# Performance work log

Hardware: AMD Instinct MI355X
Metric: run time of the kernel (lower is better)

Reference implementation:

```python
import jax, jax.numpy as jnp
import numpy as np

# Gemma3-style config
B, S, HID = 2, 2048, 2560      # 2 sequences of 2048 tokens (flattened ragged prefill, equal lengths)
H, KV, D = 8, 4, 256           # attention heads, kv heads (GQA groups=2), head_dim
WINDOW = 1024                  # sliding window (is_sliding=True)
EPS = 1e-6
SCALE = 256.0 ** -0.5          # query_pre_attn_scalar ** -0.5
ROPE_BASE = 10000.0            # rope_local_base_freq for sliding layers


def setup_inputs() -> dict:
    key = jax.random.key(0)
    ks = jax.random.split(key, 5)
    T = B * S
    hidden_states = jax.random.normal(ks[0], (T, HID), jnp.float32)
    # real rotary tables: positions restart per sequence
    inv_freq = 1.0 / (ROPE_BASE ** (np.arange(0, D, 2, dtype=np.float64) / D))  # [D/2]
    pos = np.tile(np.arange(S, dtype=np.float64), B)                             # [T]
    ang = pos[:, None] * inv_freq[None, :]                                       # [T, D/2]
    cos = jnp.asarray(np.cos(ang), jnp.float32)
    sin = jnp.asarray(np.sin(ang), jnp.float32)
    w_qkv = jax.random.normal(ks[1], ((H + 2 * KV) * D, HID), jnp.float32) * 0.02
    q_norm_w = 1.0 + jax.random.normal(ks[2], (D,), jnp.float32) * 0.02  # Gemma stores weight-1, loads +1
    k_norm_w = 1.0 + jax.random.normal(ks[3], (D,), jnp.float32) * 0.02
    w_o = jax.random.normal(ks[4], (HID, H * D), jnp.float32) * 0.02
    return dict(hidden_states=hidden_states, cos=cos, sin=sin, w_qkv=w_qkv,
                q_norm_w=q_norm_w, k_norm_w=k_norm_w, w_o=w_o)


def _rmsnorm(x, w):
    # per-head RMSNorm in fp32, as Gemma3FastRMSNorm. x: [T, h, D]
    xf = x.astype(jnp.float32)
    var = jnp.mean(xf * xf, axis=-1, keepdims=True)
    return (xf * jax.lax.rsqrt(var + EPS) * w).astype(x.dtype)


def _rope(x, cos, sin):
    # neox-style rotary: rotate across head_dim halves. x: [T, h, D]; cos/sin: [T, D/2]
    x1, x2 = x[..., : D // 2], x[..., D // 2:]
    c, s = cos[:, None, :], sin[:, None, :]
    return jnp.concatenate([x1 * c - x2 * s, x2 * c + x1 * s], axis=-1)


def reference(hidden_states, cos, sin, w_qkv, q_norm_w, k_norm_w, w_o):
    T = hidden_states.shape[0]
    qkv = hidden_states @ w_qkv.T                              # [T, (H+2KV)*D]
    q = qkv[:, : H * D].reshape(T, H, D)
    k = qkv[:, H * D: (H + KV) * D].reshape(T, KV, D)
    v = qkv[:, (H + KV) * D:].reshape(T, KV, D)
    q = _rmsnorm(q, q_norm_w)
    k = _rmsnorm(k, k_norm_w)
    q = _rope(q, cos, sin)
    k = _rope(k, cos, sin)
    # unflatten ragged tokens into [B, S, h, D] (equal-length prefill)
    qb = q.reshape(B, S, H, D)
    kb = jnp.repeat(k.reshape(B, S, KV, D), H // KV, axis=2)   # GQA expand
    vb = jnp.repeat(v.reshape(B, S, KV, D), H // KV, axis=2)
    scores = jnp.einsum('bqhd,bkhd->bhqk', qb, kb) * SCALE     # [B, H, S, S]
    i = jnp.arange(S)[:, None]
    j = jnp.arange(S)[None, :]
    mask = (j <= i) & ((i - j) < WINDOW)                       # causal + sliding window
    scores = jnp.where(mask, scores, jnp.float32(-1e30))
    p = jax.nn.softmax(scores, axis=-1)
    attn = jnp.einsum('bhqk,bkhd->bqhd', p, vb)                # [B, S, H, D]
    attn = attn.reshape(T, H * D)
    return attn @ w_o.T                                        # [T, HID]
```

## Files before the change

### kernel.cpp

```cpp
#include <hip/hip_runtime.h>
#include <cstdint>
#include <cstddef>

#define T_TOK 4096
#define HIDDIM 2560
#define NH 8
#define NKV 4
#define HD 256
#define SEQ 2048
#define NBATCH 2
#define WIN 1024
#define NQKV 4096
#define QSCALE 0.0625f

typedef unsigned short u16;
typedef __attribute__((ext_vector_type(8))) __bf16 bf16x8;
typedef __attribute__((ext_vector_type(8))) u16 u16x8;
typedef __attribute__((ext_vector_type(4))) float f32x4;

__device__ __forceinline__ u16 f2bf(float f) {
  union { float f; uint32_t u; } x{f};
  uint32_t r = x.u + 0x7FFFu + ((x.u >> 16) & 1u);
  return (u16)(r >> 16);
}
__device__ __forceinline__ float bf2f(u16 h) {
  union { uint32_t u; float f; } x{((uint32_t)h) << 16};
  return x.f;
}
__device__ __forceinline__ void gload_lds16(const void* g, void* l) {
  __builtin_amdgcn_global_load_lds((const __attribute__((address_space(1))) unsigned int*)g,
                                   (__attribute__((address_space(3))) unsigned int*)l, 16, 0, 0);
}
template <int N>
__device__ __forceinline__ void vmcnt_wait() {
  if constexpr (N >= 8) asm volatile("s_waitcnt vmcnt(8)" ::: "memory");
  else if constexpr (N == 6) asm volatile("s_waitcnt vmcnt(6)" ::: "memory");
  else if constexpr (N == 4) asm volatile("s_waitcnt vmcnt(4)" ::: "memory");
  else if constexpr (N == 3) asm volatile("s_waitcnt vmcnt(3)" ::: "memory");
  else asm volatile("s_waitcnt vmcnt(0)" ::: "memory");
}

__global__ void cvt_bf16(const float* __restrict__ in, u16* __restrict__ out, int n8) {
  int i = blockIdx.x * 256 + threadIdx.x;
  if (i >= n8) return;
  const f32x4* p = (const f32x4*)(in + (size_t)i * 8);
  f32x4 a = p[0], b = p[1];
  u16 o[8];
  o[0] = f2bf(a[0]); o[1] = f2bf(a[1]); o[2] = f2bf(a[2]); o[3] = f2bf(a[3]);
  o[4] = f2bf(b[0]); o[5] = f2bf(b[1]); o[6] = f2bf(b[2]); o[7] = f2bf(b[3]);
  *(u16x8*)(out + (size_t)i * 8) = *(const u16x8*)o;
}

template <int M, int N, int K, int BN, int OUTBF16>
__global__ __launch_bounds__(512, 2) void gemm256(const u16* __restrict__ A,
                                                  const u16* __restrict__ Bt,
                                                  void* __restrict__ Cp) {
  constexpr int NT = K / 32;
  constexpr int BCH = BN * 4;
  constexpr int LPT = (1024 + BCH) / 512;
  constexpr int NREP = BN / 64;
  constexpr int BUFB = 16384 + BN * 64;
  __shared__ char smem[4 * BUFB];

  const int tid = threadIdx.x, lane = tid & 63, w = tid >> 6;
  const int wr = w >> 2, wc = w & 3, hi = lane >> 4, lo = lane & 15;
  const int hi16 = hi * 16;
  constexpr int TOT = (M / 256) * (N / BN);
  const int bid = blockIdx.x;
  const int wg = (bid & 7) * (TOT / 8) + (bid >> 3);
  const int m0 = (wg / (N / BN)) * 256;
  const int n0 = (wg % (N / BN)) * BN;

  f32x4 acc[8][NREP] = {};

  auto stage = [&](int tt, int bb) {
    const int k0 = tt * 32;
    char* base = smem + bb * BUFB;
#pragma unroll
    for (int it = 0; it < 2; ++it) {
      int c = tid + it * 512;
      int r = (c >> 2) ^ ((c >> 4) & 1);
      int h = (c & 3) ^ (r & 3);
      gload_lds16(A + (size_t)(m0 + r) * K + k0 + h * 8, base + c * 16);
    }
#pragma unroll
    for (int it = 0; it < BCH / 512; ++it) {
      int c = tid + it * 512;
      int r = (c >> 2) ^ ((c >> 4) & 1);
      int h = (c & 3) ^ (r & 3);
      gload_lds16(Bt + (size_t)(n0 + r) * K + k0 + h * 8, base + 16384 + c * 16);
    }
  };
  auto body = [&](int bb) {
    char* base = smem + bb * BUFB;
    bf16x8 a[8], b[NREP];
#pragma unroll
    for (int mi = 0; mi < 8; ++mi) {
      int r = wr * 128 + mi * 16 + lo;
      a[mi] = *(const bf16x8*)(base + ((r * 64 + hi16) ^ ((r & 7) << 4)));
    }
#pragma unroll
    for (int ni = 0; ni < NREP; ++ni) {
      int r = wc * (BN / 4) + ni * 16 + lo;
      b[ni] = *(const bf16x8*)(base + 16384 + ((r * 64 + hi16) ^ ((r & 7) << 4)));
    }
    __builtin_amdgcn_s_setprio(1);
#pragma unroll
    for (int mi = 0; mi < 8; ++mi)
#pragma unroll
      for (int ni = 0; ni < NREP; ++ni)
        acc[mi][ni] = __builtin_amdgcn_mfma_f32_16x16x32_bf16(a[mi], b[ni], acc[mi][ni], 0, 0, 0);
    __builtin_amdgcn_s_setprio(0);
  };

  stage(0, 0); stage(1, 1); stage(2, 2);
  vmcnt_wait<2 * LPT>();
  __builtin_amdgcn_s_barrier();
  int t = 0;
  for (; t < NT - 3; ++t) {
    stage(t + 3, (t + 3) & 3);
    body(t & 3);
    vmcnt_wait<2 * LPT>();
    __builtin_amdgcn_s_barrier();
  }
  body(t & 3); vmcnt_wait<LPT>(); __builtin_amdgcn_s_barrier(); ++t;
  body(t & 3); vmcnt_wait<0>();   __builtin_amdgcn_s_barrier(); ++t;
  body(t & 3);

#pragma unroll
  for (int mi = 0; mi < 8; ++mi)
#pragma unroll
    for (int ni = 0; ni < NREP; ++ni) {
      int row = m0 + wr * 128 + mi * 16 + hi * 4;
      int col = n0 + wc * (BN / 4) + ni * 16 + lo;
#pragma unroll
      for (int r = 0; r < 4; ++r) {
        if (OUTBF16)
          ((u16*)Cp)[(size_t)(row + r) * N + col] = f2bf(acc[mi][ni][r]);
        else
          ((float*)Cp)[(size_t)(row + r) * N + col] = acc[mi][ni][r];
      }
    }
}

__global__ void norm_rope(const u16* __restrict__ qkv, const float* __restrict__ cosb,
                          const float* __restrict__ sinb, const float* __restrict__ qw,
                          const float* __restrict__ kw, u16* __restrict__ qn,
                          u16* __restrict__ kn) {
  int gw = blockIdx.x * 4 + (threadIdx.x >> 6);
  int lane = threadIdx.x & 63;
  int t = gw / 12, hh = gw % 12;
  const u16* x = qkv + (size_t)t * NQKV + hh * HD;
  int d = lane * 2;
  float x1a = bf2f(x[d]), x1b = bf2f(x[d + 1]);
  float x2a = bf2f(x[d + 128]), x2b = bf2f(x[d + 129]);
  float ss = x1a * x1a + x1b * x1b + x2a * x2a + x2b * x2b;
#pragma unroll
  for (int off = 1; off < 64; off <<= 1) ss += __shfl_xor(ss, off, 64);
  float inv = rsqrtf(ss * (1.0f / 256.0f) + 1e-6f);
  const float* wp = (hh < 8) ? qw : kw;
  float c0 = cosb[t * 128 + d], c1 = cosb[t * 128 + d + 1];
  float s0 = sinb[t * 128 + d], s1 = sinb[t * 128 + d + 1];
  float sc = (hh < 8) ? QSCALE : 1.0f;
  float y1a = x1a * inv * wp[d], y1b = x1b * inv * wp[d + 1];
  float y2a = x2a * inv * wp[d + 128], y2b = x2b * inv * wp[d + 129];
  float o1a = (y1a * c0 - y2a * s0) * sc, o1b = (y1b * c1 - y2b * s1) * sc;
  float o2a = (y2a * c0 + y1a * s0) * sc, o2b = (y2b * c1 + y1b * s1) * sc;
  u16* o = (hh < 8) ? (qn + ((size_t)t * 8 + hh) * HD) : (kn + ((size_t)t * 4 + (hh - 8)) * HD);
  ushort2 lo2, hi2;
  lo2.x = f2bf(o1a); lo2.y = f2bf(o1b);
  hi2.x = f2bf(o2a); hi2.y = f2bf(o2b);
  *(ushort2*)&o[d] = lo2;
  *(ushort2*)&o[d + 128] = hi2;
}

__global__ void vtransp(const u16* __restrict__ qkv, u16* __restrict__ vt) {
  const int b = blockIdx.y >> 2, kv = blockIdx.y & 3;
  const int s0 = blockIdx.x * 64;
  const int t = threadIdx.x;
  __shared__ u16 tile[64 * 64];
  for (int d0 = 0; d0 < 256; d0 += 64) {
#pragma unroll
    for (int it = 0; it < 2; ++it) {
      int c = t + it * 256;
      int sr = c >> 3, dc = (c & 7) * 8;
      bf16x8 v = *(const bf16x8*)&qkv[(size_t)(b * SEQ + s0 + sr) * NQKV + 3072 + kv * HD + d0 + dc];
      *(bf16x8*)((char*)tile + ((sr * 128 + dc * 2) ^ ((sr & 7) << 4))) = v;
    }
    __syncthreads();
#pragma unroll
    for (int it = 0; it < 2; ++it) {
      int c = t + it * 256;
      int dr = c >> 3, sc0 = (c & 7) * 8;
      union { u16 a[8]; bf16x8 v; } u;
#pragma unroll
      for (int j = 0; j < 8; ++j) {
        int s = sc0 + j;
        u.a[j] = *(const u16*)((char*)tile + ((s * 128 + dr * 2) ^ ((s & 7) << 4)));
      }
      *(bf16x8*)&vt[((size_t)(b * 4 + kv) * 256 + d0 + dr) * SEQ + s0 + sc0] = u.v;
    }
    __syncthreads();
  }
}

__global__ __launch_bounds__(256, 2) void attn_fwd(const u16* __restrict__ qn,
                                                   const u16* __restrict__ kn,
                                                   const u16* __restrict__ vt,
                                                   u16* __restrict__ aout) {
  const int qt = blockIdx.x * 64, h = blockIdx.y, b = blockIdx.z;
  const int kvh = h >> 1;
  const int t = threadIdx.x, lane = t & 63, w = t >> 6, hi = lane >> 4, lo = lane & 15;
  __shared__ u16 Ks[32 * 256];
  __shared__ u16 Vs[256 * 32];
  __shared__ u16 Ps[4][16 * 32];
  bf16x8 qf[8];
  const int qrow = qt + w * 16 + lo;
#pragma unroll
  for (int dd = 0; dd < 8; ++dd)
    qf[dd] = *(const bf16x8*)&qn[((size_t)(b * SEQ + qrow) * 8 + h) * HD + dd * 32 + hi * 8];
  f32x4 oacc[16] = {};
  float mrow[4] = {-3e38f, -3e38f, -3e38f, -3e38f};
  float lrow[4] = {0.f, 0.f, 0.f, 0.f};
  const int kstart = qt >= WIN ? qt - WIN : 0;
  const int irow = qt + w * 16 + hi * 4;
  for (int kt = kstart; kt < qt + 64; kt += 32) {
#pragma unroll
    for (int it = 0; it < 4; ++it) {
      int c = t + it * 256;
      int kr = c >> 5, dc = (c & 31) * 8;
      bf16x8 val = *(const bf16x8*)&kn[((size_t)(b * SEQ + kt + kr) * 4 + kvh) * HD + dc];
      *(bf16x8*)((char*)Ks + ((kr * 512 + dc * 2) ^ ((kr & 7) << 4))) = val;
    }
#pragma unroll
    for (int it = 0; it < 4; ++it) {
      int c = t + it * 256;
      int dr = c >> 2, kc = (c & 3) * 8;
      bf16x8 val = *(const bf16x8*)&vt[((size_t)(b * 4 + kvh) * 256 + dr) * SEQ + kt + kc];
      *(bf16x8*)((char*)Vs + ((dr * 64 + kc * 2) ^ ((dr & 7) << 4))) = val;
    }
    __syncthreads();
    f32x4 sacc[2];
#pragma unroll
    for (int kk = 0; kk < 2; ++kk) {
      f32x4 sa = {0.f, 0.f, 0.f, 0.f};
#pragma unroll
      for (int dd = 0; dd < 8; ++dd) {
        int krow = kk * 16 + lo;
        bf16x8 kf = *(const bf16x8*)((char*)Ks + ((krow * 512 + (dd * 32 + hi * 8) * 2) ^ ((krow & 7) << 4)));
        sa = __builtin_amdgcn_mfma_f32_16x16x32_bf16(qf[dd], kf, sa, 0, 0, 0);
      }
      sacc[kk] = sa;
    }
    float pe[2][4];
    float tmax[4] = {-3e38f, -3e38f, -3e38f, -3e38f};
#pragma unroll
    for (int kk = 0; kk < 2; ++kk)
#pragma unroll
      for (int r = 0; r < 4; ++r) {
        int i = irow + r, j = kt + kk * 16 + lo;
        bool ok = (j <= i) && (i - j < WIN);
        float sv = ok ? sacc[kk][r] : -3e38f;
        sacc[kk][r] = sv;
        tmax[r] = fmaxf(tmax[r], sv);
      }
#pragma unroll
    for (int off = 1; off < 16; off <<= 1)
#pragma unroll
      for (int r = 0; r < 4; ++r) tmax[r] = fmaxf(tmax[r], __shfl_xor(tmax[r], off, 64));
    float scl[4], tsum[4];
#pragma unroll
    for (int r = 0; r < 4; ++r) {
      float mnew = fmaxf(mrow[r], tmax[r]);
      scl[r] = __expf(mrow[r] - mnew);
      mrow[r] = mnew;
      tsum[r] = 0.f;
    }
#pragma unroll
    for (int kk = 0; kk < 2; ++kk)
#pragma unroll
      for (int r = 0; r < 4; ++r) {
        float sv = sacc[kk][r];
        float p = (sv <= -1e37f) ? 0.f : __expf(sv - mrow[r]);
        pe[kk][r] = p;
        tsum[r] += p;
      }
#pragma unroll
    for (int off = 1; off < 16; off <<= 1)
#pragma unroll
      for (int r = 0; r < 4; ++r) tsum[r] += __shfl_xor(tsum[r], off, 64);
#pragma unroll
    for (int r = 0; r < 4; ++r) lrow[r] = lrow[r] * scl[r] + tsum[r];
#pragma unroll
    for (int dt = 0; dt < 16; ++dt)
#pragma unroll
      for (int r = 0; r < 4; ++r) oacc[dt][r] *= scl[r];
#pragma unroll
    for (int kk = 0; kk < 2; ++kk)
#pragma unroll
      for (int r = 0; r < 4; ++r) {
        int q = hi * 4 + r, cc = kk * 16 + lo;
        *(u16*)((char*)&Ps[w][0] + ((q * 64 + cc * 2) ^ ((q & 7) << 4))) = f2bf(pe[kk][r]);
      }
    bf16x8 pf = *(const bf16x8*)((char*)&Ps[w][0] + ((lo * 64 + hi * 16) ^ ((lo & 7) << 4)));
#pragma unroll
    for (int dt = 0; dt < 16; ++dt) {
      int d = dt * 16 + lo;
      bf16x8 vf = *(const bf16x8*)((char*)Vs + ((d * 64 + hi * 16) ^ ((d & 7) << 4)));
      oacc[dt] = __builtin_amdgcn_mfma_f32_16x16x32_bf16(pf, vf, oacc[dt], 0, 0, 0);
    }
    __syncthreads();
  }
#pragma unroll
  for (int dt = 0; dt < 16; ++dt)
#pragma unroll
    for (int r = 0; r < 4; ++r) {
      int i = irow + r;
      aout[(size_t)(b * SEQ + i) * 2048 + h * HD + dt * 16 + lo] = f2bf(oacc[dt][r] / lrow[r]);
    }
}

extern "C" void kernel_launch(void* const* d_in, const int* in_sizes, int n_in,
                              void* d_out, int out_size, void* d_ws, size_t ws_size,
                              hipStream_t stream) {
  const float* hs = (const float*)d_in[0];
  const float* cosb = (const float*)d_in[1];
  const float* sinb = (const float*)d_in[2];
  const float* wqkv = (const float*)d_in[3];
  const float* qw = (const float*)d_in[4];
  const float* kw = (const float*)d_in[5];
  const float* wo = (const float*)d_in[6];
  char* ws = (char*)d_ws;
  u16* hs_b = (u16*)(ws);
  u16* wqkv_b = (u16*)(ws + 20971520);
  u16* wo_b = (u16*)(ws + 41943040);
  u16* qkv_b = (u16*)(ws + 52428800);
  u16* kn = (u16*)(ws + 85983232);
  u16* vt = (u16*)(ws + 94371840);
  u16* qn = wqkv_b;
  u16* attn = hs_b;

  cvt_bf16<<<5120, 256, 0, stream>>>(hs, hs_b, 1310720);
  cvt_bf16<<<5120, 256, 0, stream>>>(wqkv, wqkv_b, 1310720);
  cvt_bf16<<<2560, 256, 0, stream>>>(wo, wo_b, 655360);
  gemm256<4096, 4096, 2560, 256, 1><<<256, 512, 0, stream>>>(hs_b, wqkv_b, qkv_b);
  norm_rope<<<12288, 256, 0, stream>>>(qkv_b, cosb, sinb, qw, kw, qn, kn);
  vtransp<<<dim3(32, 8), 256, 0, stream>>>(qkv_b, vt);
  attn_fwd<<<dim3(32, 8, 2), 256, 0, stream>>>(qn, kn, vt, attn);
  gemm256<4096, 2560, 2048, 128, 0><<<320, 512, 0, stream>>>(attn, wo_b, d_out);
}
```

Baseline: 423.9 us.

## Double the attention KV tile and prefetch next tile through registers

The attention kernel now processes 64 keys per iteration instead of 32, which halves the number of loop iterations and barriers. The next K/V tile is loaded from global memory into registers while the current tile's MFMAs run, then written to LDS between two barriers. Masking is applied only on the diagonal and window-edge tiles. The cost is higher register pressure (kreg/vreg plus larger score arrays) and doubled LDS use, which may lower occupancy under launch_bounds(256,2).

```diff
diff --git a/kernel.cpp b/kernel.cpp
--- a/kernel.cpp
+++ b/kernel.cpp
@@ -211,59 +211,90 @@
   const int qt = blockIdx.x * 64, h = blockIdx.y, b = blockIdx.z;
   const int kvh = h >> 1;
   const int t = threadIdx.x, lane = t & 63, w = t >> 6, hi = lane >> 4, lo = lane & 15;
-  __shared__ u16 Ks[32 * 256];
-  __shared__ u16 Vs[256 * 32];
-  __shared__ u16 Ps[4][16 * 32];
+  __shared__ u16 Ks[64 * 256];
+  __shared__ u16 Vs[256 * 64];
+  __shared__ u16 Ps[4][16 * 64];
+
   bf16x8 qf[8];
   const int qrow = qt + w * 16 + lo;
 #pragma unroll
   for (int dd = 0; dd < 8; ++dd)
     qf[dd] = *(const bf16x8*)&qn[((size_t)(b * SEQ + qrow) * 8 + h) * HD + dd * 32 + hi * 8];
+
   f32x4 oacc[16] = {};
   float mrow[4] = {-3e38f, -3e38f, -3e38f, -3e38f};
   float lrow[4] = {0.f, 0.f, 0.f, 0.f};
   const int kstart = qt >= WIN ? qt - WIN : 0;
   const int irow = qt + w * 16 + hi * 4;
-  for (int kt = kstart; kt < qt + 64; kt += 32) {
-#pragma unroll
-    for (int it = 0; it < 4; ++it) {
+
+  bf16x8 kreg[8], vreg[8];
+  auto ldK = [&](int kt2) {
+#pragma unroll
+    for (int it = 0; it < 8; ++it) {
       int c = t + it * 256;
-      int kr = c >> 5, dc = (c & 31) * 8;
-      bf16x8 val = *(const bf16x8*)&kn[((size_t)(b * SEQ + kt + kr) * 4 + kvh) * HD + dc];
-      *(bf16x8*)((char*)Ks + ((kr * 512 + dc * 2) ^ ((kr & 7) << 4))) = val;
-    }
-#pragma unroll
-    for (int it = 0; it < 4; ++it) {
+      kreg[it] = *(const bf16x8*)&kn[((size_t)(b * SEQ + kt2 + (c >> 5)) * 4 + kvh) * HD + (c & 31) * 8];
+    }
+  };
+  auto ldV = [&](int kt2) {
+#pragma unroll
+    for (int it = 0; it < 8; ++it) {
       int c = t + it * 256;
-      int dr = c >> 2, kc = (c & 3) * 8;
-      bf16x8 val = *(const bf16x8*)&vt[((size_t)(b * 4 + kvh) * 256 + dr) * SEQ + kt + kc];
-      *(bf16x8*)((char*)Vs + ((dr * 64 + kc * 2) ^ ((dr & 7) << 4))) = val;
-    }
-    __syncthreads();
-    f32x4 sacc[2];
-#pragma unroll
-    for (int kk = 0; kk < 2; ++kk) {
+      vreg[it] = *(const bf16x8*)&vt[((size_t)(b * 4 + kvh) * 256 + (c >> 3)) * SEQ + kt2 + (c & 7) * 8];
+    }
+  };
+  auto stK = [&]() {
+#pragma unroll
+    for (int it = 0; it < 8; ++it) {
+      int c = t + it * 256, kr = c >> 5;
+      *(bf16x8*)((char*)Ks + ((kr * 512 + (c & 31) * 16) ^ ((kr & 7) << 4))) = kreg[it];
+    }
+  };
+  auto stV = [&]() {
+#pragma unroll
+    for (int it = 0; it < 8; ++it) {
+      int c = t + it * 256, dr = c >> 3;
+      *(bf16x8*)((char*)Vs + ((dr * 128 + (c & 7) * 16) ^ ((dr & 7) << 4))) = vreg[it];
+    }
+  };
+
+  ldK(kstart); ldV(kstart);
+  stK(); stV();
+  __syncthreads();
+
+  for (int kt = kstart; kt <= qt; kt += 64) {
+    f32x4 sacc[4];
+#pragma unroll
+    for (int kk = 0; kk < 4; ++kk) {
       f32x4 sa = {0.f, 0.f, 0.f, 0.f};
+      int krow = kk * 16 + lo;
 #pragma unroll
       for (int dd = 0; dd < 8; ++dd) {
-        int krow = kk * 16 + lo;
         bf16x8 kf = *(const bf16x8*)((char*)Ks + ((krow * 512 + (dd * 32 + hi * 8) * 2) ^ ((krow & 7) << 4)));
         sa = __builtin_amdgcn_mfma_f32_16x16x32_bf16(qf[dd], kf, sa, 0, 0, 0);
       }
       sacc[kk] = sa;
     }
-    float pe[2][4];
+    const bool more = (kt + 64) <= qt;
+    if (more) { ldK(kt + 64); ldV(kt + 64); }
+    const bool needmask = (kt == qt) || (qt >= WIN && kt == kstart);
     float tmax[4] = {-3e38f, -3e38f, -3e38f, -3e38f};
-#pragma unroll
-    for (int kk = 0; kk < 2; ++kk)
-#pragma unroll
-      for (int r = 0; r < 4; ++r) {
-        int i = irow + r, j = kt + kk * 16 + lo;
-        bool ok = (j <= i) && (i - j < WIN);
-        float sv = ok ? sacc[kk][r] : -3e38f;
-        sacc[kk][r] = sv;
-        tmax[r] = fmaxf(tmax[r], sv);
-      }
+    if (needmask) {
+#pragma unroll
+      for (int kk = 0; kk < 4; ++kk)
+#pragma unroll
+        for (int r = 0; r < 4; ++r) {
+          int i = irow + r, j = kt + kk * 16 + lo;
+          bool ok = (j <= i) && (i - j < WIN);
+          float sv = ok ? sacc[kk][r] : -3e38f;
+          sacc[kk][r] = sv;
+          tmax[r] = fmaxf(tmax[r], sv);
+        }
+    } else {
+#pragma unroll
+      for (int kk = 0; kk < 4; ++kk)
+#pragma unroll
+        for (int r = 0; r < 4; ++r) tmax[r] = fmaxf(tmax[r], sacc[kk][r]);
+    }
 #pragma unroll
     for (int off = 1; off < 16; off <<= 1)
 #pragma unroll
@@ -276,8 +307,9 @@
       mrow[r] = mnew;
       tsum[r] = 0.f;
     }
-#pragma unroll
-    for (int kk = 0; kk < 2; ++kk)
+    float pe[4][4];
+#pragma unroll
+    for (int kk = 0; kk < 4; ++kk)
 #pragma unroll
       for (int r = 0; r < 4; ++r) {
         float sv = sacc[kk][r];
@@ -296,20 +328,27 @@
 #pragma unroll
       for (int r = 0; r < 4; ++r) oacc[dt][r] *= scl[r];
 #pragma unroll
-    for (int kk = 0; kk < 2; ++kk)
+    for (int kk = 0; kk < 4; ++kk)
 #pragma unroll
       for (int r = 0; r < 4; ++r) {
         int q = hi * 4 + r, cc = kk * 16 + lo;
-        *(u16*)((char*)&Ps[w][0] + ((q * 64 + cc * 2) ^ ((q & 7) << 4))) = f2bf(pe[kk][r]);
-      }
-    bf16x8 pf = *(const bf16x8*)((char*)&Ps[w][0] + ((lo * 64 + hi * 16) ^ ((lo & 7) << 4)));
+        *(u16*)((char*)&Ps[w][0] + ((q * 128 + cc * 2) ^ ((q & 7) << 4))) = f2bf(pe[kk][r]);
+      }
+    bf16x8 pf0 = *(const bf16x8*)((char*)&Ps[w][0] + ((lo * 128 + (hi * 8) * 2) ^ ((lo & 7) << 4)));
+    bf16x8 pf1 = *(const bf16x8*)((char*)&Ps[w][0] + ((lo * 128 + (32 + hi * 8) * 2) ^ ((lo & 7) << 4)));
 #pragma unroll
     for (int dt = 0; dt < 16; ++dt) {
       int d = dt * 16 + lo;
-      bf16x8 vf = *(const bf16x8*)((char*)Vs + ((d * 64 + hi * 16) ^ ((d & 7) << 4)));
-      oacc[dt] = __builtin_amdgcn_mfma_f32_16x16x32_bf16(pf, vf, oacc[dt], 0, 0, 0);
-    }
-    __syncthreads();
+      bf16x8 vf0 = *(const bf16x8*)((char*)Vs + ((d * 128 + (hi * 8) * 2) ^ ((d & 7) << 4)));
+      bf16x8 vf1 = *(const bf16x8*)((char*)Vs + ((d * 128 + (32 + hi * 8) * 2) ^ ((d & 7) << 4)));
+      oacc[dt] = __builtin_amdgcn_mfma_f32_16x16x32_bf16(pf0, vf0, oacc[dt], 0, 0, 0);
+      oacc[dt] = __builtin_amdgcn_mfma_f32_16x16x32_bf16(pf1, vf1, oacc[dt], 0, 0, 0);
+    }
+    if (more) {
+      __syncthreads();
+      stK(); stV();
+      __syncthreads();
+    }
   }
 #pragma unroll
   for (int dt = 0; dt < 16; ++dt)
```

New measurement: 615.3 us. +45.2%, slower.

## Double-buffer K/V tiles in attention with direct global-to-LDS async loads

Applied to the files above, without the earlier changes.

The attention kernel now keeps two LDS buffers for K and V. It prefetches the next 32-key tile with direct global-to-LDS 16-byte loads while the current tile runs through the QK and PV MFMAs, which drops one barrier per iteration. The XOR swizzle is now applied to the global source addresses, so the LDS write order stays linear and the existing swizzled read pattern still holds. This doubles the K/V LDS footprint, which may reduce occupancy, and it relies on the end-of-loop barrier to make sure the async loads have finished.

```diff
diff --git a/kernel.cpp b/kernel.cpp
--- a/kernel.cpp
+++ b/kernel.cpp
@@ -211,43 +211,56 @@
   const int qt = blockIdx.x * 64, h = blockIdx.y, b = blockIdx.z;
   const int kvh = h >> 1;
   const int t = threadIdx.x, lane = t & 63, w = t >> 6, hi = lane >> 4, lo = lane & 15;
-  __shared__ u16 Ks[32 * 256];
-  __shared__ u16 Vs[256 * 32];
+  __shared__ u16 Ks[2][32 * 256];
+  __shared__ u16 Vs[2][256 * 32];
   __shared__ u16 Ps[4][16 * 32];
+
   bf16x8 qf[8];
   const int qrow = qt + w * 16 + lo;
 #pragma unroll
   for (int dd = 0; dd < 8; ++dd)
     qf[dd] = *(const bf16x8*)&qn[((size_t)(b * SEQ + qrow) * 8 + h) * HD + dd * 32 + hi * 8];
+
   f32x4 oacc[16] = {};
   float mrow[4] = {-3e38f, -3e38f, -3e38f, -3e38f};
   float lrow[4] = {0.f, 0.f, 0.f, 0.f};
   const int kstart = qt >= WIN ? qt - WIN : 0;
   const int irow = qt + w * 16 + hi * 4;
+
+  auto stage = [&](int kt2, int bb) {
+#pragma unroll
+    for (int it = 0; it < 4; ++it) {
+      int s = t + it * 256;
+      int kr = s >> 5, ch = (s & 31) ^ (kr & 7);
+      gload_lds16(kn + ((size_t)(b * SEQ + kt2 + kr) * 4 + kvh) * HD + ch * 8,
+                  (char*)Ks[bb] + s * 16);
+    }
+#pragma unroll
+    for (int it = 0; it < 4; ++it) {
+      int s = t + it * 256;
+      int rp = s >> 2;
+      int dr = rp ^ ((rp >> 2) & 1);
+      int ch = (s & 3) ^ (dr & 3);
+      gload_lds16(vt + ((size_t)(b * 4 + kvh) * 256 + dr) * SEQ + kt2 + ch * 8,
+                  (char*)Vs[bb] + s * 16);
+    }
+  };
+
+  stage(kstart, 0);
+  __syncthreads();
+  int cur = 0;
+
   for (int kt = kstart; kt < qt + 64; kt += 32) {
-#pragma unroll
-    for (int it = 0; it < 4; ++it) {
-      int c = t + it * 256;
-      int kr = c >> 5, dc = (c & 31) * 8;
-      bf16x8 val = *(const bf16x8*)&kn[((size_t)(b * SEQ + kt + kr) * 4 + kvh) * HD + dc];
-      *(bf16x8*)((char*)Ks + ((kr * 512 + dc * 2) ^ ((kr & 7) << 4))) = val;
-    }
-#pragma unroll
-    for (int it = 0; it < 4; ++it) {
-      int c = t + it * 256;
-      int dr = c >> 2, kc = (c & 3) * 8;
-      bf16x8 val = *(const bf16x8*)&vt[((size_t)(b * 4 + kvh) * 256 + dr) * SEQ + kt + kc];
-      *(bf16x8*)((char*)Vs + ((dr * 64 + kc * 2) ^ ((dr & 7) << 4))) = val;
-    }
-    __syncthreads();
+    const bool more = (kt + 32) < (qt + 64);
+    if (more) stage(kt + 32, cur ^ 1);
     f32x4 sacc[2];
 #pragma unroll
     for (int kk = 0; kk < 2; ++kk) {
       f32x4 sa = {0.f, 0.f, 0.f, 0.f};
+      int krow = kk * 16 + lo;
 #pragma unroll
       for (int dd = 0; dd < 8; ++dd) {
-        int krow = kk * 16 + lo;
-        bf16x8 kf = *(const bf16x8*)((char*)Ks + ((krow * 512 + (dd * 32 + hi * 8) * 2) ^ ((krow & 7) << 4)));
+        bf16x8 kf = *(const bf16x8*)((char*)Ks[cur] + ((krow * 512 + (dd * 32 + hi * 8) * 2) ^ ((krow & 7) << 4)));
         sa = __builtin_amdgcn_mfma_f32_16x16x32_bf16(qf[dd], kf, sa, 0, 0, 0);
       }
       sacc[kk] = sa;
@@ -306,10 +319,11 @@
 #pragma unroll
     for (int dt = 0; dt < 16; ++dt) {
       int d = dt * 16 + lo;
-      bf16x8 vf = *(const bf16x8*)((char*)Vs + ((d * 64 + hi * 16) ^ ((d & 7) << 4)));
+      bf16x8 vf = *(const bf16x8*)((char*)Vs[cur] + ((d * 64 + hi * 16) ^ ((d & 7) << 4)));
       oacc[dt] = __builtin_amdgcn_mfma_f32_16x16x32_bf16(pf, vf, oacc[dt], 0, 0, 0);
     }
     __syncthreads();
+    cur ^= 1;
   }
 #pragma unroll
   for (int dt = 0; dt < 16; ++dt)
```

Result: no change. 420.4 us (-0.8%).
